# Kernel tuning notes

Measured on AMD Instinct MI355X. Metric: run time of the kernel, lower is better.

The kernel has to match this reference:

```python
import jax, jax.numpy as jnp
import numpy as np

NEG_INF = float('-inf')
POS_INF = float('inf')


def _max_pool(m, win, pad):
    # m: [N, K, D, W, H]; torch max_pool3d pads with -inf
    return jax.lax.reduce_window(m, NEG_INF, jax.lax.max,
                                 (1, 1) + win, (1, 1, 1, 1, 1),
                                 [(0, 0), (0, 0)] + pad)


def _min_pool(m, win, pad):
    # -max_pool3d(-img) with -inf pad on -img == min pool with +inf pad
    return jax.lax.reduce_window(m, POS_INF, jax.lax.min,
                                 (1, 1) + win, (1, 1, 1, 1, 1),
                                 [(0, 0), (0, 0)] + pad)


def soft_dilate(m):
    return _max_pool(m, (5, 5, 5), [(2, 2), (2, 2), (2, 2)])


def soft_erode(m):
    p1 = _min_pool(m, (5, 1, 1), [(2, 2), (0, 0), (0, 0)])
    p2 = _min_pool(m, (1, 5, 1), [(0, 0), (2, 2), (0, 0)])
    p3 = _min_pool(m, (1, 1, 5), [(0, 0), (0, 0), (2, 2)])
    return jnp.minimum(jnp.minimum(p1, p2), p3)


def setup_inputs() -> dict:
    key = jax.random.key(0)
    k1, k2 = jax.random.split(key)
    N, C, NC, D, W, H = 2, 32, 4, 96, 96, 96
    feat = jax.random.normal(k1, (N, C, D, W, H), dtype=jnp.float32)
    x = jax.random.normal(k2, (N, NC, D, W, H), dtype=jnp.float32)
    k = jnp.ones((1,), dtype=jnp.float32)
    bn_weight = jnp.ones((C,), dtype=jnp.float32)
    bn_bias = jnp.zeros((C,), dtype=jnp.float32)
    return {"feat": feat, "x": x, "k": k, "bn_weight": bn_weight, "bn_bias": bn_bias}


def reference(feat, x, k, bn_weight, bn_bias):
    N, C, D, W, H = feat.shape
    NC = x.shape[1]
    P = D * W * H
    EPS_NUM = 1e-05
    EPS_BN = 1e-05

    mask = jax.nn.sigmoid(x)                       # [N, NC, D, W, H]
    dil = soft_dilate(mask)                        # [N, NC, D, W, H]
    ero = soft_erode(mask)
    back = 1.0 - dil

    featf = feat.reshape(N, C, P)                  # [N, C, P]
    e = ero.reshape(N, NC, P)
    d = dil.reshape(N, NC, P)
    b = back.reshape(N, NC, P)

    e_sum = e.sum(-1) + EPS_NUM                    # [N, NC]
    d_sum = d.sum(-1) + EPS_NUM
    b_sum = b.sum(-1) + EPS_NUM

    ec = jnp.einsum('ncp,nkp->nkc', featf, e) / e_sum[:, :, None]   # [N, NC, C]
    dc = jnp.einsum('ncp,nkp->nkc', featf, d) / d_sum[:, :, None]
    bc = jnp.einsum('ncp,nkp->nkc', featf, b) / b_sum[:, :, None]

    fore = ec + dc
    cluster = jnp.stack([fore, bc], axis=-1)       # [N, NC, C, 2]

    sim = jnp.einsum('ncp,nkcj->nkpj', featf, cluster)   # [N, NC, P, 2]
    sim = jax.nn.softmax(sim, axis=-1)
    # sum over class axis k folded into the contraction (attn always reads feat)
    atten = jnp.einsum('nkpj,nkcj->ncp', sim, cluster)   # [N, C, P]

    # out = feat + sum_i (k*atten_i + feat) = (1+NC)*feat + k*sum_i atten_i
    out = feat * (1.0 + NC) + (k[0] * atten).reshape(N, C, D, W, H)

    # BatchNorm3d (training-mode batch statistics, biased variance)
    mean = out.mean(axis=(0, 2, 3, 4), keepdims=True)
    var = out.var(axis=(0, 2, 3, 4), keepdims=True)
    out = (out - mean) / jnp.sqrt(var + EPS_BN)
    out = out * bn_weight.reshape(1, C, 1, 1, 1) + bn_bias.reshape(1, C, 1, 1, 1)
    return out
```

## Files before the change

### kernel.cpp

```cpp
#include <hip/hip_runtime.h>

#define NN 2
#define CC 32
#define NCC 4
#define DD 96
#define WW 96
#define HH 96
#define PP (DD*WW*HH)
#define NCP (NN*NCC*PP)
#define SD (WW*HH)
#define SW HH
#define DCH (PP/2048)
#define PB  (PP/1024)
#define EPS 1e-5f
#define BIGF 1e30f

__device__ __forceinline__ float wave_reduce(float v) {
#pragma unroll
    for (int off = 32; off > 0; off >>= 1) v += __shfl_down(v, off, 64);
    return v;
}

__device__ __forceinline__ float dot8(float4 a0, float4 a1, float4 b0, float4 b1) {
    return a0.x*b0.x + a0.y*b0.y + a0.z*b0.z + a0.w*b0.w
         + a1.x*b1.x + a1.y*b1.y + a1.z*b1.z + a1.w*b1.w;
}

__device__ __forceinline__ float sigf(float v) { return 1.f / (1.f + __expf(-v)); }

__device__ __forceinline__ void max8(float4& x0, float4& x1, const float* p) {
    float4 a = *(const float4*)p, b = *(const float4*)(p + 4);
    x0.x = fmaxf(x0.x, a.x); x0.y = fmaxf(x0.y, a.y);
    x0.z = fmaxf(x0.z, a.z); x0.w = fmaxf(x0.w, a.w);
    x1.x = fmaxf(x1.x, b.x); x1.y = fmaxf(x1.y, b.y);
    x1.z = fmaxf(x1.z, b.z); x1.w = fmaxf(x1.w, b.w);
}

__device__ __forceinline__ void min8(float4& x0, float4& x1, const float* p) {
    float4 a = *(const float4*)p, b = *(const float4*)(p + 4);
    x0.x = fminf(x0.x, a.x); x0.y = fminf(x0.y, a.y);
    x0.z = fminf(x0.z, a.z); x0.w = fminf(x0.w, a.w);
    x1.x = fminf(x1.x, b.x); x1.y = fminf(x1.y, b.y);
    x1.z = fminf(x1.z, b.z); x1.w = fminf(x1.w, b.w);
}

__global__ __launch_bounds__(256) void k_poolH(const float* __restrict__ x,
                                               float* __restrict__ mask,
                                               float* __restrict__ omax) {
    int i = (blockIdx.x * 256 + threadIdx.x) * 4;
    int h0 = i % HH;
    float4 xv = *(const float4*)(x + i);
    float v0 = sigf(xv.x), v1 = sigf(xv.y), v2 = sigf(xv.z), v3 = sigf(xv.w);
    float aM = -BIGF, bM = -BIGF, cM = -BIGF, dM = -BIGF;
    if (h0 > 0)  { aM = sigf(x[i-2]); bM = sigf(x[i-1]); }
    if (h0 < 92) { cM = sigf(x[i+4]); dM = sigf(x[i+5]); }
    float4 mo = make_float4(v0, v1, v2, v3), mx;
    mx.x = fmaxf(fmaxf(aM, bM), fmaxf(fmaxf(v0, v1), v2));
    mx.y = fmaxf(bM, fmaxf(fmaxf(v0, v1), fmaxf(v2, v3)));
    mx.z = fmaxf(fmaxf(fmaxf(v0, v1), fmaxf(v2, v3)), cM);
    mx.w = fmaxf(fmaxf(v1, v2), fmaxf(v3, fmaxf(cM, dM)));
    *(float4*)(mask + i) = mo;
    *(float4*)(omax + i) = mx;
}

__global__ __launch_bounds__(256, 2) void k_pooldots(const float* __restrict__ t0,
                                                     const float* __restrict__ mask,
                                                     const float* __restrict__ feat,
                                                     float* __restrict__ dotp) {
    int b = blockIdx.x;
    int n = b / DCH;
    int pt = (b % DCH) * 2048 + threadIdx.x * 8;
    int d  = pt / SD;
    int w  = (pt / SW) % WW;
    int h0 = pt % HH;
    int wv = threadIdx.x >> 6, ln = threadIdx.x & 63;

    __shared__ float sacc[4][296];

    float4 e[NCC][2], dv[NCC][2];
#pragma unroll
    for (int k = 0; k < NCC; ++k) {
        const size_t off = (size_t)(n*NCC + k)*PP + pt;
        float4 mx0 = make_float4(-BIGF,-BIGF,-BIGF,-BIGF), mx1 = mx0;
#pragma unroll
        for (int dd = -2; dd <= 2; ++dd) {
            if ((unsigned)(d + dd) < DD) {
#pragma unroll
                for (int ww = -2; ww <= 2; ++ww) {
                    if ((unsigned)(w + ww) < WW)
                        max8(mx0, mx1, t0 + off + dd*SD + ww*SW);
                }
            }
        }
        float4 m0 = *(const float4*)(mask + off);
        float4 m1 = *(const float4*)(mask + off + 4);
        float l0 = BIGF, l1 = BIGF, r0 = BIGF, r1 = BIGF;
        if (h0 > 0)  { l0 = mask[off-2]; l1 = mask[off-1]; }
        if (h0 < 88) { r0 = mask[off+8]; r1 = mask[off+9]; }
        float mv0=l0, mv1=l1, mv2=m0.x, mv3=m0.y, mv4=m0.z, mv5=m0.w,
              mv6=m1.x, mv7=m1.y, mv8=m1.z, mv9=m1.w, mv10=r0, mv11=r1;
        float4 mn0, mn1;
        mn0.x = fminf(fminf(mv0,mv1), fminf(mv2, fminf(mv3,mv4)));
        mn0.y = fminf(fminf(mv1,mv2), fminf(mv3, fminf(mv4,mv5)));
        mn0.z = fminf(fminf(mv2,mv3), fminf(mv4, fminf(mv5,mv6)));
        mn0.w = fminf(fminf(mv3,mv4), fminf(mv5, fminf(mv6,mv7)));
        mn1.x = fminf(fminf(mv4,mv5), fminf(mv6, fminf(mv7,mv8)));
        mn1.y = fminf(fminf(mv5,mv6), fminf(mv7, fminf(mv8,mv9)));
        mn1.z = fminf(fminf(mv6,mv7), fminf(mv8, fminf(mv9,mv10)));
        mn1.w = fminf(fminf(mv7,mv8), fminf(mv9, fminf(mv10,mv11)));
        if (w >= 2)     min8(mn0, mn1, mask + off - 2*SW);
        if (w >= 1)     min8(mn0, mn1, mask + off -   SW);
        if (w + 1 < WW) min8(mn0, mn1, mask + off +   SW);
        if (w + 2 < WW) min8(mn0, mn1, mask + off + 2*SW);
        if (d >= 2)     min8(mn0, mn1, mask + off - 2*SD);
        if (d >= 1)     min8(mn0, mn1, mask + off -   SD);
        if (d + 1 < DD) min8(mn0, mn1, mask + off +   SD);
        if (d + 2 < DD) min8(mn0, mn1, mask + off + 2*SD);

        e[k][0] = mn0; e[k][1] = mn1;
        dv[k][0] = mx0; dv[k][1] = mx1;
        float th_e = mn0.x+mn0.y+mn0.z+mn0.w + mn1.x+mn1.y+mn1.z+mn1.w;
        float th_d = mx0.x+mx0.y+mx0.z+mx0.w + mx1.x+mx1.y+mx1.z+mx1.w;
        th_e = wave_reduce(th_e);
        th_d = wave_reduce(th_d);
        if (ln == 0) {
            sacc[wv][288 + k] = th_e;
            sacc[wv][292 + k] = th_d;
        }
    }

    const float* pf = feat + (size_t)(n*CC)*PP + pt;
    float4 fa = *(const float4*)pf;
    float4 fb = *(const float4*)(pf + 4);
    for (int c = 0; c < CC; ++c) {
        int cn = (c + 1 < CC) ? (c + 1) : c;
        const float* pn = pf + (size_t)cn*PP;
        float4 na = *(const float4*)pn;
        float4 nb = *(const float4*)(pn + 4);
        float vals[9];
#pragma unroll
        for (int k = 0; k < NCC; ++k) {
            vals[k]     = dot8(fa, fb, e[k][0],  e[k][1]);
            vals[4 + k] = dot8(fa, fb, dv[k][0], dv[k][1]);
        }
        vals[8] = fa.x+fa.y+fa.z+fa.w + fb.x+fb.y+fb.z+fb.w;
#pragma unroll
        for (int q = 0; q < 9; ++q) {
            float r = wave_reduce(vals[q]);
            if (ln == 0) sacc[wv][c*9 + q] = r;
        }
        fa = na; fb = nb;
    }
    __syncthreads();
    for (int t = threadIdx.x; t < 296; t += 256)
        dotp[(size_t)b*296 + t] = sacc[0][t] + sacc[1][t] + sacc[2][t] + sacc[3][t];
}

__global__ __launch_bounds__(320) void k_dotred1(const float* __restrict__ dotp,
                                                 float* __restrict__ dotp2) {
    int t = threadIdx.x;
    if (t >= 296) return;
    int g = blockIdx.x;
    int n = g / 27, gg = g % 27;
    const float* p = dotp + (size_t)(n*DCH + gg*16)*296 + t;
    float s = 0.f;
#pragma unroll
    for (int j = 0; j < 16; ++j) s += p[(size_t)j*296];
    dotp2[(size_t)g*296 + t] = s;
}

__global__ __launch_bounds__(320) void k_dotred2c(const float* __restrict__ dotp2,
                                                  float* __restrict__ cluster) {
    __shared__ float vals[296];
    int t = threadIdx.x;
    int n = blockIdx.x;
    if (t < 296) {
        float s = 0.f;
#pragma unroll
        for (int g = 0; g < 27; ++g) s += dotp2[((size_t)n*27 + g)*296 + t];
        vals[t] = s;
    }
    __syncthreads();
    if (t < NCC*CC) {
        int k = t >> 5, c = t & 31;
        float de = vals[c*9 + k];
        float dd = vals[c*9 + 4 + k];
        float fs = vals[c*9 + 8];
        float es = vals[288 + k] + EPS;
        float ds = vals[292 + k] + EPS;
        float bs = (float)PP - vals[292 + k] + EPS;
        cluster[((n*NCC + k)*CC + c)*2 + 0] = de/es + dd/ds;
        cluster[((n*NCC + k)*CC + c)*2 + 1] = (fs - dd)/bs;
    }
}

__global__ __launch_bounds__(256) void k_attn_stats(const float* __restrict__ feat,
                                                    const float* __restrict__ cluster,
                                                    const float* __restrict__ kptr,
                                                    float* __restrict__ w0a,
                                                    float* __restrict__ bnpart) {
    __shared__ float cl[NCC*CC*2];
    __shared__ float swp[4][CC*2];
    int b = blockIdx.x;
    int n = b / PB;
    int p0 = (b % PB) * 1024 + (threadIdx.x << 2);
    int wv = threadIdx.x >> 6, ln = threadIdx.x & 63;
    cl[threadIdx.x] = cluster[n*(NCC*CC*2) + threadIdx.x];
    __syncthreads();

    const float* fb = feat + (size_t)n*CC*PP + p0;

    float4 s0[NCC], s1[NCC];
#pragma unroll
    for (int k = 0; k < NCC; ++k) {
        s0[k] = make_float4(0.f, 0.f, 0.f, 0.f);
        s1[k] = make_float4(0.f, 0.f, 0.f, 0.f);
    }
    float4 fv = *(const float4*)fb;
    for (int c = 0; c < CC; ++c) {
        int cn = (c + 1 < CC) ? (c + 1) : c;
        float4 nv = *(const float4*)(fb + (size_t)cn*PP);
#pragma unroll
        for (int k = 0; k < NCC; ++k) {
            float2 cc2 = *(const float2*)&cl[(k*CC + c)*2];
            s0[k].x += fv.x*cc2.x; s0[k].y += fv.y*cc2.x;
            s0[k].z += fv.z*cc2.x; s0[k].w += fv.w*cc2.x;
            s1[k].x += fv.x*cc2.y; s1[k].y += fv.y*cc2.y;
            s1[k].z += fv.z*cc2.y; s1[k].w += fv.w*cc2.y;
        }
        fv = nv;
    }
    float4 w0[NCC], w1[NCC];
#pragma unroll
    for (int k = 0; k < NCC; ++k) {
        w0[k].x = 1.f/(1.f + __expf(s1[k].x - s0[k].x));
        w0[k].y = 1.f/(1.f + __expf(s1[k].y - s0[k].y));
        w0[k].z = 1.f/(1.f + __expf(s1[k].z - s0[k].z));
        w0[k].w = 1.f/(1.f + __expf(s1[k].w - s0[k].w));
        w1[k].x = 1.f - w0[k].x; w1[k].y = 1.f - w0[k].y;
        w1[k].z = 1.f - w0[k].z; w1[k].w = 1.f - w0[k].w;
        *(float4*)(w0a + (size_t)(n*NCC + k)*PP + p0) = w0[k];
    }

    float kk = kptr[0];
#pragma unroll 8
    for (int c = 0; c < CC; ++c) {
        float4 f2 = *(const float4*)(fb + (size_t)c*PP);
        float4 a = make_float4(0.f, 0.f, 0.f, 0.f);
#pragma unroll
        for (int k = 0; k < NCC; ++k) {
            float2 cc2 = *(const float2*)&cl[(k*CC + c)*2];
            a.x += w0[k].x*cc2.x + w1[k].x*cc2.y;
            a.y += w0[k].y*cc2.x + w1[k].y*cc2.y;
            a.z += w0[k].z*cc2.x + w1[k].z*cc2.y;
            a.w += w0[k].w*cc2.x + w1[k].w*cc2.y;
        }
        float4 o;
        o.x = 5.f*f2.x + kk*a.x; o.y = 5.f*f2.y + kk*a.y;
        o.z = 5.f*f2.z + kk*a.z; o.w = 5.f*f2.w + kk*a.w;
        float ls = o.x + o.y + o.z + o.w;
        float lq = o.x*o.x + o.y*o.y + o.z*o.z + o.w*o.w;
        ls = wave_reduce(ls);
        lq = wave_reduce(lq);
        if (ln == 0) { swp[wv][2*c] = ls; swp[wv][2*c + 1] = lq; }
    }
    __syncthreads();
    if (threadIdx.x < CC*2)
        bnpart[(size_t)b*(CC*2) + threadIdx.x] =
            swp[0][threadIdx.x] + swp[1][threadIdx.x] +
            swp[2][threadIdx.x] + swp[3][threadIdx.x];
}

__global__ __launch_bounds__(256) void k_bnred(const float* __restrict__ bnpart,
                                               const float* __restrict__ wgt,
                                               const float* __restrict__ bias,
                                               float* __restrict__ scale,
                                               float* __restrict__ shift) {
    int c = blockIdx.x;
    float s = 0.f, q = 0.f;
    for (int b = threadIdx.x; b < NN*PB; b += 256) {
        s += bnpart[(size_t)b*(CC*2) + c*2];
        q += bnpart[(size_t)b*(CC*2) + c*2 + 1];
    }
    s = wave_reduce(s); q = wave_reduce(q);
    __shared__ float a[4], bb[4];
    if ((threadIdx.x & 63) == 0) { a[threadIdx.x >> 6] = s; bb[threadIdx.x >> 6] = q; }
    __syncthreads();
    if (threadIdx.x == 0) {
        float ts = a[0]+a[1]+a[2]+a[3];
        float tq = bb[0]+bb[1]+bb[2]+bb[3];
        float inv_n = 1.f / (float)((size_t)NN * PP);
        float mean = ts * inv_n;
        float var  = tq * inv_n - mean*mean;
        float inv  = 1.f / sqrtf(var + EPS);
        float sc = wgt[c] * inv;
        scale[c] = sc;
        shift[c] = bias[c] - mean*sc;
    }
}

__global__ __launch_bounds__(256) void k_attn_apply(const float* __restrict__ feat,
                                                    const float* __restrict__ w0a,
                                                    const float* __restrict__ cluster,
                                                    const float* __restrict__ kptr,
                                                    const float* __restrict__ scale,
                                                    const float* __restrict__ shift,
                                                    float* __restrict__ out) {
    __shared__ float cl[NCC*CC*2];
    __shared__ float ssc[CC], ssh[CC];
    int b = blockIdx.x;
    int n = b / PB;
    int p0 = (b % PB) * 1024 + (threadIdx.x << 2);
    cl[threadIdx.x] = cluster[n*(NCC*CC*2) + threadIdx.x];
    if (threadIdx.x < CC) {
        ssc[threadIdx.x] = scale[threadIdx.x];
        ssh[threadIdx.x] = shift[threadIdx.x];
    }
    __syncthreads();

    float4 w0[NCC], w1[NCC];
#pragma unroll
    for (int k = 0; k < NCC; ++k) {
        w0[k] = *(const float4*)(w0a + (size_t)(n*NCC + k)*PP + p0);
        w1[k].x = 1.f - w0[k].x; w1[k].y = 1.f - w0[k].y;
        w1[k].z = 1.f - w0[k].z; w1[k].w = 1.f - w0[k].w;
    }

    float kk = kptr[0];
    const float* fb = feat + (size_t)n*CC*PP + p0;
    float* ob = out + (size_t)n*CC*PP + p0;
    float4 fv = *(const float4*)fb;
    for (int c = 0; c < CC; ++c) {
        int cn = (c + 1 < CC) ? (c + 1) : c;
        float4 nv = *(const float4*)(fb + (size_t)cn*PP);
        float4 a = make_float4(0.f, 0.f, 0.f, 0.f);
#pragma unroll
        for (int k = 0; k < NCC; ++k) {
            float2 cc2 = *(const float2*)&cl[(k*CC + c)*2];
            a.x += w0[k].x*cc2.x + w1[k].x*cc2.y;
            a.y += w0[k].y*cc2.x + w1[k].y*cc2.y;
            a.z += w0[k].z*cc2.x + w1[k].z*cc2.y;
            a.w += w0[k].w*cc2.x + w1[k].w*cc2.y;
        }
        float sc = ssc[c], sh = ssh[c];
        float4 o;
        o.x = (5.f*fv.x + kk*a.x)*sc + sh;
        o.y = (5.f*fv.y + kk*a.y)*sc + sh;
        o.z = (5.f*fv.z + kk*a.z)*sc + sh;
        o.w = (5.f*fv.w + kk*a.w)*sc + sh;
        *(float4*)(ob + (size_t)c*PP) = o;
        fv = nv;
    }
}

extern "C" void kernel_launch(void* const* d_in, const int* in_sizes, int n_in,
                              void* d_out, int out_size, void* d_ws, size_t ws_size,
                              hipStream_t stream) {
    const float* feat = (const float*)d_in[0];
    const float* x    = (const float*)d_in[1];
    const float* kp   = (const float*)d_in[2];
    const float* bnw  = (const float*)d_in[3];
    const float* bnb  = (const float*)d_in[4];
    float* out = (float*)d_out;
    float* ws  = (float*)d_ws;

    float* mask    = ws;
    float* t0      = ws + 1*(size_t)NCP;
    float* w0a     = ws + 2*(size_t)NCP;
    float* scratch = ws + 3*(size_t)NCP;
    float* dotp    = scratch;
    float* dotp2   = scratch + 262144;
    float* bnpart  = scratch + 280000;
    float* acc     = scratch + 393216;
    float* cluster = acc;
    float* scale   = acc + 512;
    float* shift   = acc + 544;

    k_poolH     <<<NCP/1024, 256, 0, stream>>>(x, mask, t0);
    k_pooldots  <<<NN*DCH, 256, 0, stream>>>(t0, mask, feat, dotp);
    k_dotred1   <<<NN*27, 320, 0, stream>>>(dotp, dotp2);
    k_dotred2c  <<<NN, 320, 0, stream>>>(dotp2, cluster);
    k_attn_stats<<<NN*PB, 256, 0, stream>>>(feat, cluster, kp, w0a, bnpart);
    k_bnred     <<<CC, 256, 0, stream>>>(bnpart, bnw, bnb, scale, shift);
    k_attn_apply<<<NN*PB, 256, 0, stream>>>(feat, w0a, cluster, kp, scale, shift, out);
}
```

Measured before the change: 333.9 us.

## Stage pooled masks in LDS and split channel dot products across waves

The pool+dot kernel now handles 1024 points per block with 4 points per thread, instead of 2048 points with 8 per thread. It writes the eroded and dilated masks to shared memory, then gives each wave 8 channels to reduce over all 1024 points. Before, every thread looped over all 32 channels and did 9 wave reductions per channel. The change cuts wave-reduction work per point, lowers register pressure and doubles the block count, at the cost of 32KB of LDS per block and twice as many partials for the follow-up reductions.

New measurement: 389.3 us. +16.6%, slower.

```diff
diff --git a/kernel.cpp b/kernel.cpp
--- a/kernel.cpp
+++ b/kernel.cpp
@@ -10,7 +10,7 @@
 #define NCP (NN*NCC*PP)
 #define SD (WW*HH)
 #define SW HH
-#define DCH (PP/2048)
+#define NCH (PP/1024)
 #define PB  (PP/1024)
 #define EPS 1e-5f
 #define BIGF 1e30f
@@ -21,27 +21,22 @@
     return v;
 }
 
-__device__ __forceinline__ float dot8(float4 a0, float4 a1, float4 b0, float4 b1) {
-    return a0.x*b0.x + a0.y*b0.y + a0.z*b0.z + a0.w*b0.w
-         + a1.x*b1.x + a1.y*b1.y + a1.z*b1.z + a1.w*b1.w;
+__device__ __forceinline__ float dot4(float4 a, float4 b) {
+    return a.x*b.x + a.y*b.y + a.z*b.z + a.w*b.w;
 }
 
 __device__ __forceinline__ float sigf(float v) { return 1.f / (1.f + __expf(-v)); }
 
-__device__ __forceinline__ void max8(float4& x0, float4& x1, const float* p) {
-    float4 a = *(const float4*)p, b = *(const float4*)(p + 4);
-    x0.x = fmaxf(x0.x, a.x); x0.y = fmaxf(x0.y, a.y);
-    x0.z = fmaxf(x0.z, a.z); x0.w = fmaxf(x0.w, a.w);
-    x1.x = fmaxf(x1.x, b.x); x1.y = fmaxf(x1.y, b.y);
-    x1.z = fmaxf(x1.z, b.z); x1.w = fmaxf(x1.w, b.w);
-}
-
-__device__ __forceinline__ void min8(float4& x0, float4& x1, const float* p) {
-    float4 a = *(const float4*)p, b = *(const float4*)(p + 4);
-    x0.x = fminf(x0.x, a.x); x0.y = fminf(x0.y, a.y);
-    x0.z = fminf(x0.z, a.z); x0.w = fminf(x0.w, a.w);
-    x1.x = fminf(x1.x, b.x); x1.y = fminf(x1.y, b.y);
-    x1.z = fminf(x1.z, b.z); x1.w = fminf(x1.w, b.w);
+__device__ __forceinline__ void max4v(float4& x, const float* p) {
+    float4 a = *(const float4*)p;
+    x.x = fmaxf(x.x, a.x); x.y = fmaxf(x.y, a.y);
+    x.z = fmaxf(x.z, a.z); x.w = fmaxf(x.w, a.w);
+}
+
+__device__ __forceinline__ void min4v(float4& x, const float* p) {
+    float4 a = *(const float4*)p;
+    x.x = fminf(x.x, a.x); x.y = fminf(x.y, a.y);
+    x.z = fminf(x.z, a.z); x.w = fminf(x.w, a.w);
 }
 
 __global__ __launch_bounds__(256) void k_poolH(const float* __restrict__ x,
@@ -63,97 +58,98 @@
     *(float4*)(omax + i) = mx;
 }
 
-__global__ __launch_bounds__(256, 2) void k_pooldots(const float* __restrict__ t0,
-                                                     const float* __restrict__ mask,
-                                                     const float* __restrict__ feat,
-                                                     float* __restrict__ dotp) {
+__global__ __launch_bounds__(256) void k_pooldots(const float* __restrict__ t0,
+                                                  const float* __restrict__ mask,
+                                                  const float* __restrict__ feat,
+                                                  float* __restrict__ dotp) {
+    __shared__ __align__(16) float sE[NCC][1024];
+    __shared__ __align__(16) float sD[NCC][1024];
+    __shared__ float sacc[296];
+    __shared__ float swp[4][8];
     int b = blockIdx.x;
-    int n = b / DCH;
-    int pt = (b % DCH) * 2048 + threadIdx.x * 8;
+    int n = b / NCH;
+    int base = (b % NCH) * 1024;
+    int t = threadIdx.x;
+    int wv = t >> 6, ln = t & 63;
+    int pt = base + t * 4;
     int d  = pt / SD;
     int w  = (pt / SW) % WW;
     int h0 = pt % HH;
-    int wv = threadIdx.x >> 6, ln = threadIdx.x & 63;
-
-    __shared__ float sacc[4][296];
-
-    float4 e[NCC][2], dv[NCC][2];
+
+    float th_e[NCC], th_d[NCC];
 #pragma unroll
     for (int k = 0; k < NCC; ++k) {
         const size_t off = (size_t)(n*NCC + k)*PP + pt;
-        float4 mx0 = make_float4(-BIGF,-BIGF,-BIGF,-BIGF), mx1 = mx0;
+        float4 mx = make_float4(-BIGF,-BIGF,-BIGF,-BIGF);
 #pragma unroll
         for (int dd = -2; dd <= 2; ++dd) {
             if ((unsigned)(d + dd) < DD) {
 #pragma unroll
                 for (int ww = -2; ww <= 2; ++ww) {
                     if ((unsigned)(w + ww) < WW)
-                        max8(mx0, mx1, t0 + off + dd*SD + ww*SW);
+                        max4v(mx, t0 + off + dd*SD + ww*SW);
                 }
             }
         }
         float4 m0 = *(const float4*)(mask + off);
-        float4 m1 = *(const float4*)(mask + off + 4);
         float l0 = BIGF, l1 = BIGF, r0 = BIGF, r1 = BIGF;
         if (h0 > 0)  { l0 = mask[off-2]; l1 = mask[off-1]; }
-        if (h0 < 88) { r0 = mask[off+8]; r1 = mask[off+9]; }
-        float mv0=l0, mv1=l1, mv2=m0.x, mv3=m0.y, mv4=m0.z, mv5=m0.w,
-              mv6=m1.x, mv7=m1.y, mv8=m1.z, mv9=m1.w, mv10=r0, mv11=r1;
-        float4 mn0, mn1;
-        mn0.x = fminf(fminf(mv0,mv1), fminf(mv2, fminf(mv3,mv4)));
-        mn0.y = fminf(fminf(mv1,mv2), fminf(mv3, fminf(mv4,mv5)));
-        mn0.z = fminf(fminf(mv2,mv3), fminf(mv4, fminf(mv5,mv6)));
-        mn0.w = fminf(fminf(mv3,mv4), fminf(mv5, fminf(mv6,mv7)));
-        mn1.x = fminf(fminf(mv4,mv5), fminf(mv6, fminf(mv7,mv8)));
-        mn1.y = fminf(fminf(mv5,mv6), fminf(mv7, fminf(mv8,mv9)));
-        mn1.z = fminf(fminf(mv6,mv7), fminf(mv8, fminf(mv9,mv10)));
-        mn1.w = fminf(fminf(mv7,mv8), fminf(mv9, fminf(mv10,mv11)));
-        if (w >= 2)     min8(mn0, mn1, mask + off - 2*SW);
-        if (w >= 1)     min8(mn0, mn1, mask + off -   SW);
-        if (w + 1 < WW) min8(mn0, mn1, mask + off +   SW);
-        if (w + 2 < WW) min8(mn0, mn1, mask + off + 2*SW);
-        if (d >= 2)     min8(mn0, mn1, mask + off - 2*SD);
-        if (d >= 1)     min8(mn0, mn1, mask + off -   SD);
-        if (d + 1 < DD) min8(mn0, mn1, mask + off +   SD);
-        if (d + 2 < DD) min8(mn0, mn1, mask + off + 2*SD);
-
-        e[k][0] = mn0; e[k][1] = mn1;
-        dv[k][0] = mx0; dv[k][1] = mx1;
-        float th_e = mn0.x+mn0.y+mn0.z+mn0.w + mn1.x+mn1.y+mn1.z+mn1.w;
-        float th_d = mx0.x+mx0.y+mx0.z+mx0.w + mx1.x+mx1.y+mx1.z+mx1.w;
-        th_e = wave_reduce(th_e);
-        th_d = wave_reduce(th_d);
-        if (ln == 0) {
-            sacc[wv][288 + k] = th_e;
-            sacc[wv][292 + k] = th_d;
-        }
-    }
-
-    const float* pf = feat + (size_t)(n*CC)*PP + pt;
-    float4 fa = *(const float4*)pf;
-    float4 fb = *(const float4*)(pf + 4);
-    for (int c = 0; c < CC; ++c) {
-        int cn = (c + 1 < CC) ? (c + 1) : c;
-        const float* pn = pf + (size_t)cn*PP;
-        float4 na = *(const float4*)pn;
-        float4 nb = *(const float4*)(pn + 4);
-        float vals[9];
-#pragma unroll
-        for (int k = 0; k < NCC; ++k) {
-            vals[k]     = dot8(fa, fb, e[k][0],  e[k][1]);
-            vals[4 + k] = dot8(fa, fb, dv[k][0], dv[k][1]);
-        }
-        vals[8] = fa.x+fa.y+fa.z+fa.w + fb.x+fb.y+fb.z+fb.w;
+        if (h0 < 92) { r0 = mask[off+4]; r1 = mask[off+5]; }
+        float4 mn;
+        mn.x = fminf(fminf(l0, l1),  fminf(m0.x, fminf(m0.y, m0.z)));
+        mn.y = fminf(l1, fminf(fminf(m0.x, m0.y), fminf(m0.z, m0.w)));
+        mn.z = fminf(fminf(m0.x, m0.y), fminf(m0.z, fminf(m0.w, r0)));
+        mn.w = fminf(fminf(m0.y, m0.z), fminf(m0.w, fminf(r0, r1)));
+        if (w >= 2)     min4v(mn, mask + off - 2*SW);
+        if (w >= 1)     min4v(mn, mask + off -   SW);
+        if (w + 1 < WW) min4v(mn, mask + off +   SW);
+        if (w + 2 < WW) min4v(mn, mask + off + 2*SW);
+        if (d >= 2)     min4v(mn, mask + off - 2*SD);
+        if (d >= 1)     min4v(mn, mask + off -   SD);
+        if (d + 1 < DD) min4v(mn, mask + off +   SD);
+        if (d + 2 < DD) min4v(mn, mask + off + 2*SD);
+
+        *(float4*)&sE[k][t*4] = mn;
+        *(float4*)&sD[k][t*4] = mx;
+        th_e[k] = mn.x + mn.y + mn.z + mn.w;
+        th_d[k] = mx.x + mx.y + mx.z + mx.w;
+    }
+#pragma unroll
+    for (int k = 0; k < NCC; ++k) { th_e[k] = wave_reduce(th_e[k]); th_d[k] = wave_reduce(th_d[k]); }
+    if (ln == 0) {
+#pragma unroll
+        for (int k = 0; k < NCC; ++k) { swp[wv][k] = th_e[k]; swp[wv][4+k] = th_d[k]; }
+    }
+    __syncthreads();
+    if (t < 8) sacc[288 + t] = swp[0][t] + swp[1][t] + swp[2][t] + swp[3][t];
+
+    const float* pf = feat + ((size_t)(n*CC) + wv*8)*PP + base;
+    for (int cl = 0; cl < 8; ++cl) {
+        float a[9];
+#pragma unroll
+        for (int q = 0; q < 9; ++q) a[q] = 0.f;
+#pragma unroll
+        for (int j = 0; j < 4; ++j) {
+            int po = j*256 + ln*4;
+            float4 fv = *(const float4*)(pf + (size_t)cl*PP + po);
+#pragma unroll
+            for (int k = 0; k < NCC; ++k) {
+                float4 e4 = *(const float4*)&sE[k][po];
+                float4 d4 = *(const float4*)&sD[k][po];
+                a[k]     += dot4(fv, e4);
+                a[4 + k] += dot4(fv, d4);
+            }
+            a[8] += fv.x + fv.y + fv.z + fv.w;
+        }
 #pragma unroll
         for (int q = 0; q < 9; ++q) {
-            float r = wave_reduce(vals[q]);
-            if (ln == 0) sacc[wv][c*9 + q] = r;
-        }
-        fa = na; fb = nb;
-    }
-    __syncthreads();
-    for (int t = threadIdx.x; t < 296; t += 256)
-        dotp[(size_t)b*296 + t] = sacc[0][t] + sacc[1][t] + sacc[2][t] + sacc[3][t];
+            float r = wave_reduce(a[q]);
+            if (ln == 0) sacc[(wv*8 + cl)*9 + q] = r;
+        }
+    }
+    __syncthreads();
+    for (int i = t; i < 296; i += 256)
+        dotp[(size_t)b*296 + i] = sacc[i];
 }
 
 __global__ __launch_bounds__(320) void k_dotred1(const float* __restrict__ dotp,
@@ -162,10 +158,10 @@
     if (t >= 296) return;
     int g = blockIdx.x;
     int n = g / 27, gg = g % 27;
-    const float* p = dotp + (size_t)(n*DCH + gg*16)*296 + t;
+    const float* p = dotp + (size_t)(n*NCH + gg*32)*296 + t;
     float s = 0.f;
 #pragma unroll
-    for (int j = 0; j < 16; ++j) s += p[(size_t)j*296];
+    for (int j = 0; j < 32; ++j) s += p[(size_t)j*296];
     dotp2[(size_t)g*296 + t] = s;
 }
 
@@ -369,15 +365,15 @@
     float* w0a     = ws + 2*(size_t)NCP;
     float* scratch = ws + 3*(size_t)NCP;
     float* dotp    = scratch;
-    float* dotp2   = scratch + 262144;
-    float* bnpart  = scratch + 280000;
-    float* acc     = scratch + 393216;
+    float* dotp2   = scratch + 524288;
+    float* bnpart  = scratch + 540672;
+    float* acc     = scratch + 655360;
     float* cluster = acc;
     float* scale   = acc + 512;
     float* shift   = acc + 544;
 
     k_poolH     <<<NCP/1024, 256, 0, stream>>>(x, mask, t0);
-    k_pooldots  <<<NN*DCH, 256, 0, stream>>>(t0, mask, feat, dotp);
+    k_pooldots  <<<NN*NCH, 256, 0, stream>>>(t0, mask, feat, dotp);
     k_dotred1   <<<NN*27, 320, 0, stream>>>(dotp, dotp2);
     k_dotred2c  <<<NN, 320, 0, stream>>>(dotp2, cluster);
     k_attn_stats<<<NN*PB, 256, 0, stream>>>(feat, cluster, kp, w0a, bnpart);
```
